# Performance work log

Hardware: AMD Instinct MI355X
Metric: run time of the kernel (lower is better)

## Reference

```python
import jax, jax.numpy as jnp
import numpy as np

N, E, G = 50000, 400000, 64
F_IN, HID, HEADS, GF, NCLS = 16, 128, 4, 10, 6


def _init(k, shape, fan):
    return jax.random.normal(k, shape, jnp.float32) * (1.0 / np.sqrt(fan))


def setup_inputs() -> dict:
    key = jax.random.key(0)
    ks = jax.random.split(key, 16)
    x = jax.random.normal(ks[0], (N, F_IN), jnp.float32)
    edge_index = jax.random.randint(ks[1], (2, E), 0, N)
    batch = jnp.sort(jax.random.randint(ks[2], (N,), 0, G))
    graph_feat = jax.random.normal(ks[3], (G, GF), jnp.float32)
    # GATConv 1: in=16 -> heads=4, out=128, concat
    W1 = _init(ks[4], (F_IN, HEADS * HID), F_IN)
    att_src1 = _init(ks[5], (HEADS, HID), HID)
    att_dst1 = _init(ks[6], (HEADS, HID), HID)
    b1 = jnp.zeros((HEADS * HID,), jnp.float32)
    # GATConv 2: in=512 -> heads=1, out=128, mean (concat=False)
    W2 = _init(ks[7], (HEADS * HID, HID), HEADS * HID)
    att_src2 = _init(ks[8], (1, HID), HID)
    att_dst2 = _init(ks[9], (1, HID), HID)
    b2 = jnp.zeros((HID,), jnp.float32)
    # graph_proj MLP 10->32->32
    Wg1 = _init(ks[10], (GF, 32), GF); bg1 = jnp.zeros((32,), jnp.float32)
    Wg2 = _init(ks[11], (32, 32), 32); bg2 = jnp.zeros((32,), jnp.float32)
    # classifier 160->128->6
    Wc1 = _init(ks[12], (HID + 32, 128), HID + 32); bc1 = jnp.zeros((128,), jnp.float32)
    Wc2 = _init(ks[13], (128, NCLS), 128); bc2 = jnp.zeros((NCLS,), jnp.float32)
    return dict(x=x, edge_index=edge_index, batch=batch, graph_feat=graph_feat,
                W1=W1, att_src1=att_src1, att_dst1=att_dst1, b1=b1,
                W2=W2, att_src2=att_src2, att_dst2=att_dst2, b2=b2,
                Wg1=Wg1, bg1=bg1, Wg2=Wg2, bg2=bg2,
                Wc1=Wc1, bc1=bc1, Wc2=Wc2, bc2=bc2)


def gat_layer(x, W, att_src, att_dst, bias, src, dst, n_nodes, heads, out_dim, concat):
    # Linear transform: [N, H, C]
    h = (x @ W).reshape(n_nodes, heads, out_dim)
    a_src = jnp.einsum('nhc,hc->nh', h, att_src)  # [N,H]
    a_dst = jnp.einsum('nhc,hc->nh', h, att_dst)  # [N,H]
    e = jax.nn.leaky_relu(a_src[src] + a_dst[dst], 0.2)  # [Etot,H]
    # segment softmax over edges grouped by dst (self-loops ensure nonempty)
    m = jax.ops.segment_max(e, dst, num_segments=n_nodes)
    ex = jnp.exp(e - m[dst])
    denom = jax.ops.segment_sum(ex, dst, num_segments=n_nodes)
    alpha = ex / denom[dst]  # [Etot,H]
    out = jax.ops.segment_sum(alpha[:, :, None] * h[src], dst, num_segments=n_nodes)  # [N,H,C]
    if concat:
        out = out.reshape(n_nodes, heads * out_dim)
    else:
        out = out.mean(axis=1)
    return out + bias


def reference(x, edge_index, batch, graph_feat,
              W1, att_src1, att_dst1, b1,
              W2, att_src2, att_dst2, b2,
              Wg1, bg1, Wg2, bg2, Wc1, bc1, Wc2, bc2):
    n = x.shape[0]
    loops = jnp.arange(n, dtype=edge_index.dtype)
    src = jnp.concatenate([edge_index[0], loops])
    dst = jnp.concatenate([edge_index[1], loops])
    h = jax.nn.elu(gat_layer(x, W1, att_src1, att_dst1, b1, src, dst, n, HEADS, HID, True))
    h = jax.nn.elu(gat_layer(h, W2, att_src2, att_dst2, b2, src, dst, n, 1, HID, False))
    # global mean pool over graphs
    g = graph_feat.shape[0]
    sums = jax.ops.segment_sum(h, batch, num_segments=g)
    counts = jax.ops.segment_sum(jnp.ones((n, 1), h.dtype), batch, num_segments=g)
    pooled = sums / jnp.maximum(counts, 1.0)
    gf = jax.nn.relu(graph_feat @ Wg1 + bg1) @ Wg2 + bg2
    z = jnp.concatenate([pooled, gf], axis=1)
    z = jax.nn.relu(z @ Wc1 + bc1)
    return z @ Wc2 + bc2
```

## Files before the change

### kernel.cpp

```cpp
#include <hip/hip_runtime.h>
#include <hip/hip_bf16.h>

#define NN 50000
#define EE 400000
#define GG 64
#define CAP 48

typedef unsigned short u16;
typedef unsigned char u8;
typedef long long i64;
typedef __attribute__((ext_vector_type(8))) short bf16x8;
typedef __attribute__((ext_vector_type(4))) float f32x4;
typedef __attribute__((ext_vector_type(2))) float f32x2;

__device__ __forceinline__ float b2f(u16 u) {
    unsigned int x = ((unsigned int)u) << 16;
    return __uint_as_float(x);
}
__device__ __forceinline__ u16 f2b(float f) {
    unsigned int x = __float_as_uint(f);
    unsigned int r = x + 0x7fffu + ((x >> 16) & 1u);
    return (u16)(r >> 16);
}
__device__ __forceinline__ u8 f2fp8(float f) {
    return (u8)(__builtin_amdgcn_cvt_pk_fp8_f32(f, f, 0, false) & 0xFF);
}
__device__ __forceinline__ f32x2 fp8x2_f32(unsigned int v, bool hi) {
    return hi ? __builtin_amdgcn_cvt_pk_f32_fp8(v, true)
              : __builtin_amdgcn_cvt_pk_f32_fp8(v, false);
}
__device__ __forceinline__ float wred_sum(float v) {
    #pragma unroll
    for (int o = 32; o; o >>= 1) v += __shfl_xor(v, o, 64);
    return v;
}
__device__ __forceinline__ float lrelu(float v) { return v > 0.f ? v : 0.2f * v; }

__global__ void k_prep(const int* __restrict__ batch, int* __restrict__ deg,
                       int* __restrict__ col, int* __restrict__ gstart,
                       const float* __restrict__ W1, const float* __restrict__ as1,
                       const float* __restrict__ ad1, u16* __restrict__ W1p,
                       const float* __restrict__ W2, u8* __restrict__ W2p,
                       float* __restrict__ pooled) {
    __shared__ float asw[16][8];
    int b = blockIdx.x, t = threadIdx.x;
    if (b < 196) {
        int n = b * 256 + t;
        if (n < NN) { deg[n] = 1; col[(size_t)n * CAP] = n; }
    } else if (b == 196) {
        if (t <= GG) {
            int lo = 0, hi = NN;
            while (lo < hi) {
                int mid = (lo + hi) >> 1;
                if (batch[mid] < t) lo = mid + 1; else hi = mid;
            }
            gstart[t] = lo;
        }
    } else if (b < 453) {
        int idx = (b - 197) * 256 + t;
        int j = idx & 7;
        int l = (idx >> 3) & 63;
        int ct = idx >> 9;
        int c = ct >> 3, tt = ct & 7;
        int p = c * 32 + (l >> 4) * 8 + j;
        int lp = p >> 3, jp = p & 7;
        int chan = 128 * (lp >> 4) + 16 * jp + (lp & 15);
        int n = tt * 16 + (l & 15);
        W2p[idx] = f2fp8(W2[chan * 128 + n]);
    } else if (b == 453) {
        int pair = t >> 1, half = t & 1;
        int k = pair >> 3, h = pair & 7;
        int hd = h & 3;
        const float* att = (h >= 4) ? ad1 : as1;
        float s = 0.f;
        int c0 = half * 64;
        for (int c = c0; c < c0 + 64; c++)
            s += W1[k * 512 + hd * 128 + c] * att[hd * 128 + c];
        s += __shfl_xor(s, 1, 64);
        if (half == 0) asw[k][h] = s;
        __syncthreads();
        for (int idx = t; idx < 33 * 64 * 8; idx += 256) {
            int j = idx & 7, l = (idx >> 3) & 63, tt = idx >> 9;
            int quad = l >> 4, m = l & 15;
            int k2 = quad * 8 + j;
            float v = 0.f;
            if (k2 < 16) {
                if (tt < 32) v = W1[k2 * 512 + tt * 16 + m];
                else if (m < 8) v = asw[k2][m];
            }
            W1p[idx] = f2b(v);
        }
    } else {
        for (int i = t; i < GG * 128; i += 256) pooled[i] = 0.f;
    }
}

__global__ void k_edges(const int* __restrict__ ei, int* __restrict__ deg,
                        int* __restrict__ col) {
    int e = blockIdx.x * 256 + threadIdx.x;
    if (e < EE) {
        int s = ei[e];
        int d = ei[EE + e];
        int slot = atomicAdd(&deg[d], 1);
        if (slot < CAP) col[(size_t)d * CAP + slot] = s;
    }
}

__global__ __launch_bounds__(256) void k_gemm1(
    const float* __restrict__ x, const u16* __restrict__ W1p,
    u8* __restrict__ h1, float* __restrict__ a_src1, float* __restrict__ a_dst1) {
    int tid = threadIdx.x;
    int wave = tid >> 6, l = tid & 63;
    int quad = l >> 4, m = l & 15;
    int row0 = blockIdx.x * 64 + wave * 16;
    int arow = row0 + m;
    int arow_c = arow < NN ? arow : (NN - 1);
    bf16x8 af;
    if (quad < 2) {
        const float* xp = x + arow_c * 16 + quad * 8;
        float4 x0 = *(const float4*)(xp);
        float4 x1 = *(const float4*)(xp + 4);
        u16 tmp[8] = {f2b(x0.x), f2b(x0.y), f2b(x0.z), f2b(x0.w),
                      f2b(x1.x), f2b(x1.y), f2b(x1.z), f2b(x1.w)};
        af = *(bf16x8*)tmp;
    } else {
        af = (bf16x8){0, 0, 0, 0, 0, 0, 0, 0};
    }
    const u16* bp = W1p + l * 8;
    f32x4 acc[33];
    #pragma unroll
    for (int tt = 0; tt < 33; tt++) acc[tt] = (f32x4){0.f, 0.f, 0.f, 0.f};
    #pragma unroll
    for (int tt = 0; tt < 33; tt++) {
        bf16x8 bf = *(const bf16x8*)(bp + (size_t)tt * 512);
        acc[tt] = __builtin_amdgcn_mfma_f32_16x16x32_bf16(af, bf, acc[tt], 0, 0, 0);
    }
    #pragma unroll
    for (int r = 0; r < 4; r++) {
        int row = row0 + quad * 4 + r;
        if (row >= NN) continue;
        unsigned int d[8];
        #pragma unroll
        for (int dd = 0; dd < 8; dd++) {
            unsigned int w = __builtin_amdgcn_cvt_pk_fp8_f32(acc[4 * dd][r], acc[4 * dd + 1][r], 0, false);
            w = __builtin_amdgcn_cvt_pk_fp8_f32(acc[4 * dd + 2][r], acc[4 * dd + 3][r], w, true);
            d[dd] = w;
        }
        uint4 v0; v0.x = d[0]; v0.y = d[1]; v0.z = d[2]; v0.w = d[3];
        uint4 v1; v1.x = d[4]; v1.y = d[5]; v1.z = d[6]; v1.w = d[7];
        *(uint4*)(h1 + (size_t)row * 512 + m * 32) = v0;
        *(uint4*)(h1 + (size_t)row * 512 + m * 32 + 16) = v1;
        float v = acc[32][r];
        if (m < 4) a_src1[row * 4 + m] = v;
        else if (m < 8) a_dst1[row * 4 + (m - 4)] = v;
    }
}

__global__ __launch_bounds__(256) void k_agg1(
    const int* __restrict__ deg, const int* __restrict__ col,
    const float* __restrict__ a_src1, const float* __restrict__ a_dst1,
    const u8* __restrict__ h1, const float* __restrict__ b1,
    u8* __restrict__ h2pre) {
    __shared__ float alphaS[4][64][4];
    int t = threadIdx.x;
    int wave = t >> 6, l = t & 63;
    int n = blockIdx.x * 4 + wave;
    if (n >= NN) return;
    int dg = min(deg[n], CAP);
    int sl = (l < dg) ? col[(size_t)n * CAP + l] : 0;
    float4 ad = *(const float4*)(a_dst1 + n * 4);
    float4 as = *(const float4*)(a_src1 + (size_t)sl * 4);
    float4 e;
    e.x = __expf(lrelu(as.x + ad.x)); e.y = __expf(lrelu(as.y + ad.y));
    e.z = __expf(lrelu(as.z + ad.z)); e.w = __expf(lrelu(as.w + ad.w));
    if (l >= dg) e = (float4){0.f, 0.f, 0.f, 0.f};
    float4 inv;
    inv.x = 1.0f / wred_sum(e.x);
    inv.y = 1.0f / wred_sum(e.y);
    inv.z = 1.0f / wred_sum(e.z);
    inv.w = 1.0f / wred_sum(e.w);
    {
        float4 a4;
        a4.x = e.x * inv.x; a4.y = e.y * inv.y;
        a4.z = e.z * inv.z; a4.w = e.w * inv.w;
        *(float4*)&alphaS[wave][l][0] = a4;
    }
    int g = l >> 4, m = l & 15;
    const u8* hb = h1 + m * 32 + g * 8;
    f32x2 acc[4] = {{0.f, 0.f}, {0.f, 0.f}, {0.f, 0.f}, {0.f, 0.f}};
    int iters = (dg + 3) >> 2;
    for (int j = 0; j < iters; j++) {
        int e0 = 4 * j, e1 = 4 * j + 1, e2 = 4 * j + 2, e3 = 4 * j + 3;
        int s0 = __shfl(sl, e0), s1 = __shfl(sl, e1);
        int s2 = __shfl(sl, e2), s3 = __shfl(sl, e3);
        float a0 = alphaS[wave][e0][g], a1 = alphaS[wave][e1][g];
        float a2 = alphaS[wave][e2][g], a3 = alphaS[wave][e3][g];
        uint2 u0 = *(const uint2*)(hb + (size_t)s0 * 512);
        uint2 u1 = *(const uint2*)(hb + (size_t)s1 * 512);
        uint2 u2 = *(const uint2*)(hb + (size_t)s2 * 512);
        uint2 u3 = *(const uint2*)(hb + (size_t)s3 * 512);
        acc[0] += a0 * fp8x2_f32(u0.x, false);
        acc[1] += a0 * fp8x2_f32(u0.x, true);
        acc[2] += a0 * fp8x2_f32(u0.y, false);
        acc[3] += a0 * fp8x2_f32(u0.y, true);
        acc[0] += a1 * fp8x2_f32(u1.x, false);
        acc[1] += a1 * fp8x2_f32(u1.x, true);
        acc[2] += a1 * fp8x2_f32(u1.y, false);
        acc[3] += a1 * fp8x2_f32(u1.y, true);
        acc[0] += a2 * fp8x2_f32(u2.x, false);
        acc[1] += a2 * fp8x2_f32(u2.x, true);
        acc[2] += a2 * fp8x2_f32(u2.y, false);
        acc[3] += a2 * fp8x2_f32(u2.y, true);
        acc[0] += a3 * fp8x2_f32(u3.x, false);
        acc[1] += a3 * fp8x2_f32(u3.x, true);
        acc[2] += a3 * fp8x2_f32(u3.y, false);
        acc[3] += a3 * fp8x2_f32(u3.y, true);
    }
    float av[8] = {acc[0].x, acc[0].y, acc[1].x, acc[1].y,
                   acc[2].x, acc[2].y, acc[3].x, acc[3].y};
    const float* bb = b1 + 128 * g + m;
    float v[8];
    #pragma unroll
    for (int j = 0; j < 8; j++) {
        float w = av[j] + bb[16 * j];
        v[j] = w > 0.f ? w : __expf(w) - 1.0f;
    }
    unsigned int d0 = __builtin_amdgcn_cvt_pk_fp8_f32(v[0], v[1], 0, false);
    d0 = __builtin_amdgcn_cvt_pk_fp8_f32(v[2], v[3], d0, true);
    unsigned int d1 = __builtin_amdgcn_cvt_pk_fp8_f32(v[4], v[5], 0, false);
    d1 = __builtin_amdgcn_cvt_pk_fp8_f32(v[6], v[7], d1, true);
    uint2 ov; ov.x = d0; ov.y = d1;
    *(uint2*)(h2pre + (size_t)n * 512 + l * 8) = ov;
}

__global__ __launch_bounds__(256) void k_gemm2(
    const u8* __restrict__ h2pre, const u8* __restrict__ W2p,
    const float* __restrict__ as2, const float* __restrict__ ad2,
    u8* __restrict__ hL2, float* __restrict__ a_src2, float* __restrict__ a_dst2) {
    int t = threadIdx.x;
    int wave = t >> 6, l = t & 63;
    int quad = l >> 4, m = l & 15;
    int row0 = blockIdx.x * 64 + wave * 16;
    int arow = row0 + m;
    int arow_c = arow < NN ? arow : (NN - 1);
    const u8* aptr = h2pre + (size_t)arow_c * 512 + quad * 8;
    const u8* bptr = W2p + l * 8;
    f32x4 acc[8];
    #pragma unroll
    for (int tt = 0; tt < 8; tt++) acc[tt] = (f32x4){0.f, 0.f, 0.f, 0.f};
    for (int c = 0; c < 16; c++) {
        i64 af = *(const i64*)(aptr + c * 32);
        #pragma unroll
        for (int tt = 0; tt < 8; tt++) {
            i64 bf = *(const i64*)(bptr + (size_t)(c * 8 + tt) * 512);
            acc[tt] = __builtin_amdgcn_mfma_f32_16x16x32_fp8_fp8(af, bf, acc[tt], 0, 0, 0);
        }
    }
    float asv[8], adv[8];
    #pragma unroll
    for (int tt = 0; tt < 8; tt++) {
        int colc = tt * 16 + m;
        asv[tt] = as2[colc];
        adv[tt] = ad2[colc];
    }
    #pragma unroll
    for (int r = 0; r < 4; r++) {
        int row = row0 + quad * 4 + r;
        bool ok = row < NN;
        float rs = 0.f, rd = 0.f;
        #pragma unroll
        for (int tt = 0; tt < 8; tt++) {
            float v = acc[tt][r];
            rs += v * asv[tt];
            rd += v * adv[tt];
        }
        if (ok) {
            unsigned int d0 = __builtin_amdgcn_cvt_pk_fp8_f32(acc[0][r], acc[1][r], 0, false);
            d0 = __builtin_amdgcn_cvt_pk_fp8_f32(acc[2][r], acc[3][r], d0, true);
            unsigned int d1 = __builtin_amdgcn_cvt_pk_fp8_f32(acc[4][r], acc[5][r], 0, false);
            d1 = __builtin_amdgcn_cvt_pk_fp8_f32(acc[6][r], acc[7][r], d1, true);
            uint2 ov; ov.x = d0; ov.y = d1;
            *(uint2*)(hL2 + (size_t)row * 128 + m * 8) = ov;
        }
        #pragma unroll
        for (int o = 1; o < 16; o <<= 1) {
            rs += __shfl_xor(rs, o, 64);
            rd += __shfl_xor(rd, o, 64);
        }
        if (ok && m == 0) { a_src2[row] = rs; a_dst2[row] = rd; }
    }
}

__global__ __launch_bounds__(256) void k_agg2(
    const int* __restrict__ deg, const int* __restrict__ col,
    const float* __restrict__ a_src2, const float* __restrict__ a_dst2,
    const u8* __restrict__ hL2, const float* __restrict__ b2v,
    const int* __restrict__ batch, float* __restrict__ pooled) {
    __shared__ float red[4][128];
    __shared__ int gS[4];
    int t = threadIdx.x;
    int wave = t >> 6, l = t & 63;
    int n = blockIdx.x * 4 + wave;
    if (n >= NN) return;
    int dg = min(deg[n], CAP);
    int sl = (l < dg) ? col[(size_t)n * CAP + l] : 0;
    float ad = a_dst2[n];
    float e = (l < dg) ? __expf(lrelu(a_src2[sl] + ad)) : 0.f;
    float inv = 1.0f / wred_sum(e);
    float al = e * inv;
    f32x2 acc = {0.f, 0.f};
    const u8* hb = hL2 + l * 2;
    int iters = (dg + 3) >> 2;
    for (int j = 0; j < iters; j++) {
        int e0 = 4 * j, e1 = 4 * j + 1, e2 = 4 * j + 2, e3 = 4 * j + 3;
        int s0 = __shfl(sl, e0), s1 = __shfl(sl, e1);
        int s2 = __shfl(sl, e2), s3 = __shfl(sl, e3);
        float a0 = __shfl(al, e0), a1 = __shfl(al, e1);
        float a2 = __shfl(al, e2), a3 = __shfl(al, e3);
        unsigned int u0 = *(const u16*)(hb + (size_t)s0 * 128);
        unsigned int u1 = *(const u16*)(hb + (size_t)s1 * 128);
        unsigned int u2 = *(const u16*)(hb + (size_t)s2 * 128);
        unsigned int u3 = *(const u16*)(hb + (size_t)s3 * 128);
        acc += a0 * fp8x2_f32(u0, false);
        acc += a1 * fp8x2_f32(u1, false);
        acc += a2 * fp8x2_f32(u2, false);
        acc += a3 * fp8x2_f32(u3, false);
    }
    int c0 = ((2 * l) & 7) * 16 + (l >> 2);
    int c1 = c0 + 16;
    float o0 = acc.x + b2v[c0]; o0 = o0 > 0.f ? o0 : __expf(o0) - 1.0f;
    float o1 = acc.y + b2v[c1]; o1 = o1 > 0.f ? o1 : __expf(o1) - 1.0f;
    red[wave][c0] = o0;
    red[wave][c1] = o1;
    if (l == 0) gS[wave] = batch[n];
    __syncthreads();
    if (t < 128) {
        int g0 = gS[0];
        if (gS[1] == g0 && gS[2] == g0 && gS[3] == g0) {
            float s = red[0][t] + red[1][t] + red[2][t] + red[3][t];
            atomicAdd(&pooled[g0 * 128 + t], s);
        } else {
            #pragma unroll
            for (int w = 0; w < 4; w++)
                atomicAdd(&pooled[gS[w] * 128 + t], red[w][t]);
        }
    }
}

__global__ __launch_bounds__(128) void k_head(
    const int* __restrict__ gstart, const float* __restrict__ pooled,
    const float* __restrict__ gfeat,
    const float* __restrict__ Wg1, const float* __restrict__ bg1,
    const float* __restrict__ Wg2, const float* __restrict__ bg2,
    const float* __restrict__ Wc1, const float* __restrict__ bc1,
    const float* __restrict__ Wc2, const float* __restrict__ bc2,
    float* __restrict__ out) {
    __shared__ float z[160];
    __shared__ float hg[32];
    __shared__ float c1b[128];
    int g = blockIdx.x, t = threadIdx.x;
    float cntf = (float)(gstart[g + 1] - gstart[g]);
    z[t] = pooled[g * 128 + t] / fmaxf(cntf, 1.0f);
    if (t < 32) {
        float a = bg1[t];
        for (int i = 0; i < 10; i++) a += gfeat[g * 10 + i] * Wg1[i * 32 + t];
        hg[t] = fmaxf(a, 0.f);
    }
    __syncthreads();
    if (t < 32) {
        float a = bg2[t];
        for (int i = 0; i < 32; i++) a += hg[i] * Wg2[i * 32 + t];
        z[128 + t] = a;
    }
    __syncthreads();
    float a = bc1[t];
    for (int i = 0; i < 160; i++) a += z[i] * Wc1[i * 128 + t];
    c1b[t] = fmaxf(a, 0.f);
    __syncthreads();
    if (t < 6) {
        float o = bc2[t];
        for (int i = 0; i < 128; i++) o += c1b[i] * Wc2[i * 6 + t];
        out[g * 6 + t] = o;
    }
}

extern "C" void kernel_launch(void* const* d_in, const int* in_sizes, int n_in,
                              void* d_out, int out_size, void* d_ws, size_t ws_size,
                              hipStream_t stream) {
    const float* x     = (const float*)d_in[0];
    const int*   ei    = (const int*)d_in[1];
    const int*   batch = (const int*)d_in[2];
    const float* gfeat = (const float*)d_in[3];
    const float* W1    = (const float*)d_in[4];
    const float* as1   = (const float*)d_in[5];
    const float* ad1   = (const float*)d_in[6];
    const float* b1    = (const float*)d_in[7];
    const float* W2    = (const float*)d_in[8];
    const float* as2   = (const float*)d_in[9];
    const float* ad2   = (const float*)d_in[10];
    const float* b2    = (const float*)d_in[11];
    const float* Wg1   = (const float*)d_in[12];
    const float* bg1   = (const float*)d_in[13];
    const float* Wg2   = (const float*)d_in[14];
    const float* bg2   = (const float*)d_in[15];
    const float* Wc1   = (const float*)d_in[16];
    const float* bc1   = (const float*)d_in[17];
    const float* Wc2   = (const float*)d_in[18];
    const float* bc2   = (const float*)d_in[19];
    float* out = (float*)d_out;

    size_t off = 0;
    char* base = (char*)d_ws;
    auto take = [&](size_t nbytes) -> char* {
        char* p = base + off;
        off = (off + nbytes + 255) & ~(size_t)255;
        return p;
    };
    u8*    h1     = (u8*)take((size_t)NN * 512);
    u8*    h2pre  = (u8*)take((size_t)NN * 512);
    u8*    hL2    = (u8*)take((size_t)NN * 128);
    float* a_src1 = (float*)take((size_t)NN * 4 * 4);
    float* a_dst1 = (float*)take((size_t)NN * 4 * 4);
    float* a_src2 = (float*)take((size_t)NN * 4);
    float* a_dst2 = (float*)take((size_t)NN * 4);
    int*   deg    = (int*)take((size_t)NN * 4);
    int*   col    = (int*)take((size_t)NN * CAP * 4);
    float* pooled = (float*)take(GG * 128 * 4);
    int*   gstart = (int*)take((GG + 1) * 4);
    u8*    W2p    = (u8*)take((size_t)512 * 128);
    u16*   W1p    = (u16*)take((size_t)33 * 64 * 8 * 2);
    (void)ws_size; (void)in_sizes; (void)n_in; (void)out_size;

    k_prep<<<455, 256, 0, stream>>>(batch, deg, col, gstart, W1, as1, ad1, W1p,
                                    W2, W2p, pooled);
    k_edges<<<(EE + 255) / 256, 256, 0, stream>>>(ei, deg, col);
    k_gemm1<<<(NN + 63) / 64, 256, 0, stream>>>(x, W1p, h1, a_src1, a_dst1);
    k_agg1<<<(NN + 3) / 4, 256, 0, stream>>>(deg, col, a_src1, a_dst1, h1, b1, h2pre);
    k_gemm2<<<(NN + 63) / 64, 256, 0, stream>>>(h2pre, W2p, as2, ad2, hL2, a_src2, a_dst2);
    k_agg2<<<(NN + 3) / 4, 256, 0, stream>>>(deg, col, a_src2, a_dst2, hL2, b2,
                                             batch, pooled);
    k_head<<<GG, 128, 0, stream>>>(gstart, pooled, gfeat, Wg1, bg1, Wg2, bg2,
                                   Wc1, bc1, Wc2, bc2, out);
}
```

Before: 255.3 us.

## Fuse layer-1 aggregation with layer-2 GEMM through shared-memory row tiles

Merges the layer-1 attention aggregation and the layer-2 FP8 MFMA GEMM into one kernel. Each block aggregates 16 nodes into a padded LDS tile, then its four waves each compute two 16-column output tiles, reducing the attention logits across waves in LDS. This removes the global write and re-read of the 50000x512 intermediate and one kernel launch. In exchange the grid is 4x smaller, each wave handles four nodes serially, and each wave loads its own slice of W2 per block. The k_agg2 column mapping changes to match the new hL2 column layout.

```diff
diff --git a/kernel.cpp b/kernel.cpp
--- a/kernel.cpp
+++ b/kernel.cpp
@@ -5,10 +5,12 @@
 #define EE 400000
 #define GG 64
 #define CAP 48
+#define HROW 520
 
 typedef unsigned short u16;
 typedef unsigned char u8;
 typedef long long i64;
+typedef unsigned long long u64;
 typedef __attribute__((ext_vector_type(8))) short bf16x8;
 typedef __attribute__((ext_vector_type(4))) float f32x4;
 typedef __attribute__((ext_vector_type(2))) float f32x2;
@@ -156,138 +158,125 @@
     }
 }
 
-__global__ __launch_bounds__(256) void k_agg1(
+__global__ __launch_bounds__(256) void k_mid(
     const int* __restrict__ deg, const int* __restrict__ col,
     const float* __restrict__ a_src1, const float* __restrict__ a_dst1,
     const u8* __restrict__ h1, const float* __restrict__ b1,
-    u8* __restrict__ h2pre) {
+    const u8* __restrict__ W2p, const float* __restrict__ as2,
+    const float* __restrict__ ad2, u8* __restrict__ hL2,
+    float* __restrict__ a_src2, float* __restrict__ a_dst2) {
+    __shared__ u64 hrowq[16 * HROW / 8];
     __shared__ float alphaS[4][64][4];
+    __shared__ float part[16][2][4];
+    u8* hrow = (u8*)hrowq;
     int t = threadIdx.x;
-    int wave = t >> 6, l = t & 63;
-    int n = blockIdx.x * 4 + wave;
-    if (n >= NN) return;
-    int dg = min(deg[n], CAP);
-    int sl = (l < dg) ? col[(size_t)n * CAP + l] : 0;
-    float4 ad = *(const float4*)(a_dst1 + n * 4);
-    float4 as = *(const float4*)(a_src1 + (size_t)sl * 4);
-    float4 e;
-    e.x = __expf(lrelu(as.x + ad.x)); e.y = __expf(lrelu(as.y + ad.y));
-    e.z = __expf(lrelu(as.z + ad.z)); e.w = __expf(lrelu(as.w + ad.w));
-    if (l >= dg) e = (float4){0.f, 0.f, 0.f, 0.f};
-    float4 inv;
-    inv.x = 1.0f / wred_sum(e.x);
-    inv.y = 1.0f / wred_sum(e.y);
-    inv.z = 1.0f / wred_sum(e.z);
-    inv.w = 1.0f / wred_sum(e.w);
-    {
-        float4 a4;
-        a4.x = e.x * inv.x; a4.y = e.y * inv.y;
-        a4.z = e.z * inv.z; a4.w = e.w * inv.w;
-        *(float4*)&alphaS[wave][l][0] = a4;
-    }
+    int w = t >> 6, l = t & 63;
+    int n0 = blockIdx.x * 16;
     int g = l >> 4, m = l & 15;
     const u8* hb = h1 + m * 32 + g * 8;
-    f32x2 acc[4] = {{0.f, 0.f}, {0.f, 0.f}, {0.f, 0.f}, {0.f, 0.f}};
-    int iters = (dg + 3) >> 2;
-    for (int j = 0; j < iters; j++) {
-        int e0 = 4 * j, e1 = 4 * j + 1, e2 = 4 * j + 2, e3 = 4 * j + 3;
-        int s0 = __shfl(sl, e0), s1 = __shfl(sl, e1);
-        int s2 = __shfl(sl, e2), s3 = __shfl(sl, e3);
-        float a0 = alphaS[wave][e0][g], a1 = alphaS[wave][e1][g];
-        float a2 = alphaS[wave][e2][g], a3 = alphaS[wave][e3][g];
-        uint2 u0 = *(const uint2*)(hb + (size_t)s0 * 512);
-        uint2 u1 = *(const uint2*)(hb + (size_t)s1 * 512);
-        uint2 u2 = *(const uint2*)(hb + (size_t)s2 * 512);
-        uint2 u3 = *(const uint2*)(hb + (size_t)s3 * 512);
-        acc[0] += a0 * fp8x2_f32(u0.x, false);
-        acc[1] += a0 * fp8x2_f32(u0.x, true);
-        acc[2] += a0 * fp8x2_f32(u0.y, false);
-        acc[3] += a0 * fp8x2_f32(u0.y, true);
-        acc[0] += a1 * fp8x2_f32(u1.x, false);
-        acc[1] += a1 * fp8x2_f32(u1.x, true);
-        acc[2] += a1 * fp8x2_f32(u1.y, false);
-        acc[3] += a1 * fp8x2_f32(u1.y, true);
-        acc[0] += a2 * fp8x2_f32(u2.x, false);
-        acc[1] += a2 * fp8x2_f32(u2.x, true);
-        acc[2] += a2 * fp8x2_f32(u2.y, false);
-        acc[3] += a2 * fp8x2_f32(u2.y, true);
-        acc[0] += a3 * fp8x2_f32(u3.x, false);
-        acc[1] += a3 * fp8x2_f32(u3.x, true);
-        acc[2] += a3 * fp8x2_f32(u3.y, false);
-        acc[3] += a3 * fp8x2_f32(u3.y, true);
-    }
-    float av[8] = {acc[0].x, acc[0].y, acc[1].x, acc[1].y,
-                   acc[2].x, acc[2].y, acc[3].x, acc[3].y};
-    const float* bb = b1 + 128 * g + m;
-    float v[8];
-    #pragma unroll
-    for (int j = 0; j < 8; j++) {
-        float w = av[j] + bb[16 * j];
-        v[j] = w > 0.f ? w : __expf(w) - 1.0f;
-    }
-    unsigned int d0 = __builtin_amdgcn_cvt_pk_fp8_f32(v[0], v[1], 0, false);
-    d0 = __builtin_amdgcn_cvt_pk_fp8_f32(v[2], v[3], d0, true);
-    unsigned int d1 = __builtin_amdgcn_cvt_pk_fp8_f32(v[4], v[5], 0, false);
-    d1 = __builtin_amdgcn_cvt_pk_fp8_f32(v[6], v[7], d1, true);
-    uint2 ov; ov.x = d0; ov.y = d1;
-    *(uint2*)(h2pre + (size_t)n * 512 + l * 8) = ov;
-}
-
-__global__ __launch_bounds__(256) void k_gemm2(
-    const u8* __restrict__ h2pre, const u8* __restrict__ W2p,
-    const float* __restrict__ as2, const float* __restrict__ ad2,
-    u8* __restrict__ hL2, float* __restrict__ a_src2, float* __restrict__ a_dst2) {
-    int t = threadIdx.x;
-    int wave = t >> 6, l = t & 63;
-    int quad = l >> 4, m = l & 15;
-    int row0 = blockIdx.x * 64 + wave * 16;
-    int arow = row0 + m;
-    int arow_c = arow < NN ? arow : (NN - 1);
-    const u8* aptr = h2pre + (size_t)arow_c * 512 + quad * 8;
-    const u8* bptr = W2p + l * 8;
-    f32x4 acc[8];
-    #pragma unroll
-    for (int tt = 0; tt < 8; tt++) acc[tt] = (f32x4){0.f, 0.f, 0.f, 0.f};
+    for (int i = 0; i < 4; i++) {
+        int n = n0 + w * 4 + i;
+        int dg = min(deg[n], CAP);
+        int sl = (l < dg) ? col[(size_t)n * CAP + l] : 0;
+        float4 ad = *(const float4*)(a_dst1 + n * 4);
+        float4 as = *(const float4*)(a_src1 + (size_t)sl * 4);
+        float4 e;
+        e.x = __expf(lrelu(as.x + ad.x)); e.y = __expf(lrelu(as.y + ad.y));
+        e.z = __expf(lrelu(as.z + ad.z)); e.w = __expf(lrelu(as.w + ad.w));
+        if (l >= dg) e = (float4){0.f, 0.f, 0.f, 0.f};
+        float4 inv;
+        inv.x = 1.0f / wred_sum(e.x);
+        inv.y = 1.0f / wred_sum(e.y);
+        inv.z = 1.0f / wred_sum(e.z);
+        inv.w = 1.0f / wred_sum(e.w);
+        {
+            float4 a4;
+            a4.x = e.x * inv.x; a4.y = e.y * inv.y;
+            a4.z = e.z * inv.z; a4.w = e.w * inv.w;
+            *(float4*)&alphaS[w][l][0] = a4;
+        }
+        f32x2 acc[4] = {{0.f, 0.f}, {0.f, 0.f}, {0.f, 0.f}, {0.f, 0.f}};
+        int iters = (dg + 3) >> 2;
+        for (int j = 0; j < iters; j++) {
+            int e0 = 4 * j, e1 = 4 * j + 1, e2 = 4 * j + 2, e3 = 4 * j + 3;
+            int s0 = __shfl(sl, e0), s1 = __shfl(sl, e1);
+            int s2 = __shfl(sl, e2), s3 = __shfl(sl, e3);
+            float a0 = alphaS[w][e0][g], a1 = alphaS[w][e1][g];
+            float a2 = alphaS[w][e2][g], a3 = alphaS[w][e3][g];
+            uint2 u0 = *(const uint2*)(hb + (size_t)s0 * 512);
+            uint2 u1 = *(const uint2*)(hb + (size_t)s1 * 512);
+            uint2 u2 = *(const uint2*)(hb + (size_t)s2 * 512);
+            uint2 u3 = *(const uint2*)(hb + (size_t)s3 * 512);
+            acc[0] += a0 * fp8x2_f32(u0.x, false);
+            acc[1] += a0 * fp8x2_f32(u0.x, true);
+            acc[2] += a0 * fp8x2_f32(u0.y, false);
+            acc[3] += a0 * fp8x2_f32(u0.y, true);
+            acc[0] += a1 * fp8x2_f32(u1.x, false);
+            acc[1] += a1 * fp8x2_f32(u1.x, true);
+            acc[2] += a1 * fp8x2_f32(u1.y, false);
+            acc[3] += a1 * fp8x2_f32(u1.y, true);
+            acc[0] += a2 * fp8x2_f32(u2.x, false);
+            acc[1] += a2 * fp8x2_f32(u2.x, true);
+            acc[2] += a2 * fp8x2_f32(u2.y, false);
+            acc[3] += a2 * fp8x2_f32(u2.y, true);
+            acc[0] += a3 * fp8x2_f32(u3.x, false);
+            acc[1] += a3 * fp8x2_f32(u3.x, true);
+            acc[2] += a3 * fp8x2_f32(u3.y, false);
+            acc[3] += a3 * fp8x2_f32(u3.y, true);
+        }
+        float av[8] = {acc[0].x, acc[0].y, acc[1].x, acc[1].y,
+                       acc[2].x, acc[2].y, acc[3].x, acc[3].y};
+        const float* bb = b1 + 128 * g + m;
+        float v[8];
+        #pragma unroll
+        for (int j = 0; j < 8; j++) {
+            float q = av[j] + bb[16 * j];
+            v[j] = q > 0.f ? q : __expf(q) - 1.0f;
+        }
+        unsigned int d0 = __builtin_amdgcn_cvt_pk_fp8_f32(v[0], v[1], 0, false);
+        d0 = __builtin_amdgcn_cvt_pk_fp8_f32(v[2], v[3], d0, true);
+        unsigned int d1 = __builtin_amdgcn_cvt_pk_fp8_f32(v[4], v[5], 0, false);
+        d1 = __builtin_amdgcn_cvt_pk_fp8_f32(v[6], v[7], d1, true);
+        uint2 ov; ov.x = d0; ov.y = d1;
+        *(uint2*)(hrow + (w * 4 + i) * HROW + l * 8) = ov;
+    }
+    __syncthreads();
+    int quad = l >> 4;
+    int tt0 = 2 * w;
+    const u8* bbase = W2p + l * 8;
+    f32x4 accA = (f32x4){0.f, 0.f, 0.f, 0.f};
+    f32x4 accB = (f32x4){0.f, 0.f, 0.f, 0.f};
+    #pragma unroll
     for (int c = 0; c < 16; c++) {
-        i64 af = *(const i64*)(aptr + c * 32);
-        #pragma unroll
-        for (int tt = 0; tt < 8; tt++) {
-            i64 bf = *(const i64*)(bptr + (size_t)(c * 8 + tt) * 512);
-            acc[tt] = __builtin_amdgcn_mfma_f32_16x16x32_fp8_fp8(af, bf, acc[tt], 0, 0, 0);
-        }
-    }
-    float asv[8], adv[8];
-    #pragma unroll
-    for (int tt = 0; tt < 8; tt++) {
-        int colc = tt * 16 + m;
-        asv[tt] = as2[colc];
-        adv[tt] = ad2[colc];
-    }
+        i64 af = *(const i64*)(hrow + m * HROW + c * 32 + quad * 8);
+        i64 bf0 = *(const i64*)(bbase + (size_t)(c * 8 + tt0) * 512);
+        i64 bf1 = *(const i64*)(bbase + (size_t)(c * 8 + tt0 + 1) * 512);
+        accA = __builtin_amdgcn_mfma_f32_16x16x32_fp8_fp8(af, bf0, accA, 0, 0, 0);
+        accB = __builtin_amdgcn_mfma_f32_16x16x32_fp8_fp8(af, bf1, accB, 0, 0, 0);
+    }
+    float as0 = as2[tt0 * 16 + m], ad0 = ad2[tt0 * 16 + m];
+    float as1v = as2[(tt0 + 1) * 16 + m], ad1v = ad2[(tt0 + 1) * 16 + m];
     #pragma unroll
     for (int r = 0; r < 4; r++) {
-        int row = row0 + quad * 4 + r;
-        bool ok = row < NN;
-        float rs = 0.f, rd = 0.f;
-        #pragma unroll
-        for (int tt = 0; tt < 8; tt++) {
-            float v = acc[tt][r];
-            rs += v * asv[tt];
-            rd += v * adv[tt];
-        }
-        if (ok) {
-            unsigned int d0 = __builtin_amdgcn_cvt_pk_fp8_f32(acc[0][r], acc[1][r], 0, false);
-            d0 = __builtin_amdgcn_cvt_pk_fp8_f32(acc[2][r], acc[3][r], d0, true);
-            unsigned int d1 = __builtin_amdgcn_cvt_pk_fp8_f32(acc[4][r], acc[5][r], 0, false);
-            d1 = __builtin_amdgcn_cvt_pk_fp8_f32(acc[6][r], acc[7][r], d1, true);
-            uint2 ov; ov.x = d0; ov.y = d1;
-            *(uint2*)(hL2 + (size_t)row * 128 + m * 8) = ov;
-        }
+        int node = n0 + quad * 4 + r;
+        float v0 = accA[r], v1 = accB[r];
+        hL2[(size_t)node * 128 + tt0 * 16 + m] = f2fp8(v0);
+        hL2[(size_t)node * 128 + (tt0 + 1) * 16 + m] = f2fp8(v1);
+        float rs = v0 * as0 + v1 * as1v;
+        float rd = v0 * ad0 + v1 * ad1v;
         #pragma unroll
         for (int o = 1; o < 16; o <<= 1) {
             rs += __shfl_xor(rs, o, 64);
             rd += __shfl_xor(rd, o, 64);
         }
-        if (ok && m == 0) { a_src2[row] = rs; a_dst2[row] = rd; }
+        if (m == 0) { part[quad * 4 + r][0][w] = rs; part[quad * 4 + r][1][w] = rd; }
+    }
+    __syncthreads();
+    if (t < 32) {
+        int row = t >> 1, which = t & 1;
+        float s = part[row][which][0] + part[row][which][1] +
+                  part[row][which][2] + part[row][which][3];
+        if (which) a_dst2[n0 + row] = s; else a_src2[n0 + row] = s;
     }
 }
 
@@ -326,12 +315,10 @@
         acc += a2 * fp8x2_f32(u2, false);
         acc += a3 * fp8x2_f32(u3, false);
     }
-    int c0 = ((2 * l) & 7) * 16 + (l >> 2);
-    int c1 = c0 + 16;
-    float o0 = acc.x + b2v[c0]; o0 = o0 > 0.f ? o0 : __expf(o0) - 1.0f;
-    float o1 = acc.y + b2v[c1]; o1 = o1 > 0.f ? o1 : __expf(o1) - 1.0f;
-    red[wave][c0] = o0;
-    red[wave][c1] = o1;
+    float o0 = acc.x + b2v[2 * l];     o0 = o0 > 0.f ? o0 : __expf(o0) - 1.0f;
+    float o1 = acc.y + b2v[2 * l + 1]; o1 = o1 > 0.f ? o1 : __expf(o1) - 1.0f;
+    red[wave][2 * l] = o0;
+    red[wave][2 * l + 1] = o1;
     if (l == 0) gS[wave] = batch[n];
     __syncthreads();
     if (t < 128) {
@@ -417,7 +404,6 @@
         return p;
     };
     u8*    h1     = (u8*)take((size_t)NN * 512);
-    u8*    h2pre  = (u8*)take((size_t)NN * 512);
     u8*    hL2    = (u8*)take((size_t)NN * 128);
     float* a_src1 = (float*)take((size_t)NN * 4 * 4);
     float* a_dst1 = (float*)take((size_t)NN * 4 * 4);
@@ -435,8 +421,8 @@
                                     W2, W2p, pooled);
     k_edges<<<(EE + 255) / 256, 256, 0, stream>>>(ei, deg, col);
     k_gemm1<<<(NN + 63) / 64, 256, 0, stream>>>(x, W1p, h1, a_src1, a_dst1);
-    k_agg1<<<(NN + 3) / 4, 256, 0, stream>>>(deg, col, a_src1, a_dst1, h1, b1, h2pre);
-    k_gemm2<<<(NN + 63) / 64, 256, 0, stream>>>(h2pre, W2p, as2, ad2, hL2, a_src2, a_dst2);
+    k_mid<<<NN / 16, 256, 0, stream>>>(deg, col, a_src1, a_dst1, h1, b1,
+                                       W2p, as2, ad2, hL2, a_src2, a_dst2);
     k_agg2<<<(NN + 3) / 4, 256, 0, stream>>>(deg, col, a_src2, a_dst2, hL2, b2,
                                              batch, pooled);
     k_head<<<GG, 128, 0, stream>>>(gstart, pooled, gfeat, Wg1, bg1, Wg2, bg2,
```

Result: faster. 243.9 us (-4.5%).
